# Performance work log

Measured on AMD Instinct MI355X. Metric: run time of the kernel, lower is better.

## Reference

```python
import jax, jax.numpy as jnp
import numpy as np

EPS = 1e-5   # epsilon default in the torch wrapper
D_CKV = 512  # latent-KV channels normalized by RMSNorm
D_ROPE = 64  # rope channels written to k_cache


def setup_inputs() -> dict:
    key = jax.random.key(0)
    ks = jax.random.split(key, 5)
    B, S, L = 16, 1024, 8192
    kv = jax.random.normal(ks[0], (B, 1, S, D_CKV + D_ROPE), dtype=jnp.float32)
    gamma = jax.random.normal(ks[1], (D_CKV,), dtype=jnp.float32)
    cos = jax.random.normal(ks[2], (B, 1, S, D_ROPE), dtype=jnp.float32)
    sin = jax.random.normal(ks[3], (B, 1, S, D_ROPE), dtype=jnp.float32)
    index = jax.random.randint(ks[4], (B, S), 0, L, dtype=jnp.int32)
    k_cache = jnp.zeros((B, 1, L, D_ROPE), dtype=jnp.float32)
    ckv_cache = jnp.zeros((B, 1, L, D_CKV), dtype=jnp.float32)
    return {"kv": kv, "gamma": gamma, "cos": cos, "sin": sin,
            "index": index, "k_cache": k_cache, "ckv_cache": ckv_cache}


def reference(kv, gamma, cos, sin, index, k_cache, ckv_cache):
    # cacheMode='Norm': max_slot is the cache length dim
    B, _, S, D = kv.shape
    L = k_cache.shape[2]
    dr = k_cache.shape[3]            # 64 rope channels
    dc = D - dr                      # 512 latent channels

    idx = jnp.abs(index) % L         # [B, S], as in the torch wrapper

    ckv = kv[..., :dc]               # [B,1,S,512]
    kr = kv[..., dc:]                # [B,1,S,64]

    # RMSNorm over the 512 latent channels
    inv = jax.lax.rsqrt(jnp.mean(ckv * ckv, axis=-1, keepdims=True) + EPS)
    ckv_n = ckv * inv * gamma        # [B,1,S,512]

    # RoPE (rotate-half) on the 64 rope channels
    half = dr // 2
    rot = jnp.concatenate([-kr[..., half:], kr[..., :half]], axis=-1)
    k_r = kr * cos + rot * sin       # [B,1,S,64]

    # scatter-write each token into its cache slot (per batch)
    gidx = (jnp.arange(B, dtype=idx.dtype)[:, None] * L + idx).reshape(-1)  # [B*S]
    k_new = k_cache.reshape(B * L, dr).at[gidx].set(k_r.reshape(B * S, dr)).reshape(B, 1, L, dr)
    ckv_new = ckv_cache.reshape(B * L, dc).at[gidx].set(ckv_n.reshape(B * S, dc)).reshape(B, 1, L, dc)
    return k_new, ckv_new
```

## Files before the change

kernel.cpp:

```cpp
#include <hip/hip_runtime.h>

#define B_  16
#define S_  1024
#define L_  8192
#define DC  512
#define DR  64
#define EPSV 1e-5f

typedef float fv4 __attribute__((ext_vector_type(4)));

__global__ void owner_kernel(const int* __restrict__ index, int* __restrict__ owner) {
    int t = blockIdx.x * blockDim.x + threadIdx.x;
    if (t >= B_ * S_) return;
    int b = t >> 10;
    int s = t & (S_ - 1);
    int v = index[t];
    v = v < 0 ? -v : v;
    int idx = v & (L_ - 1);
    atomicMax(&owner[b * L_ + idx], s);
}

__global__ __launch_bounds__(256) void update_kernel(
    const float* __restrict__ kv,
    const float* __restrict__ gamma,
    const float* __restrict__ cosb,
    const float* __restrict__ sinb,
    const float* __restrict__ k_cache,
    const float* __restrict__ ckv_cache,
    const int*  __restrict__ owner,
    float* __restrict__ out_k,
    float* __restrict__ out_ckv)
{
    const int wave = threadIdx.x >> 6;
    const int lane = threadIdx.x & 63;
    const int line = (blockIdx.x << 2) + wave;
    const int o = owner[line];

    fv4*   dst_ckv = (fv4*)(out_ckv + (size_t)line * DC);
    float* dst_k   = out_k + (size_t)line * DR;

    if (o < 0) {
        const fv4* src = (const fv4*)(ckv_cache + (size_t)line * DC);
        fv4 a = __builtin_nontemporal_load(&src[lane]);
        fv4 b = __builtin_nontemporal_load(&src[lane + 64]);
        __builtin_nontemporal_store(a, &dst_ckv[lane]);
        __builtin_nontemporal_store(b, &dst_ckv[lane + 64]);
        float kc = __builtin_nontemporal_load(&k_cache[(size_t)line * DR + lane]);
        __builtin_nontemporal_store(kc, &dst_k[lane]);
        return;
    }

    const int b = line >> 13;
    const int token = b * S_ + o;
    const float* kvp = kv + (size_t)token * (DC + DR);

    fv4 c0 = __builtin_nontemporal_load(&((const fv4*)kvp)[lane]);
    fv4 c1 = __builtin_nontemporal_load(&((const fv4*)kvp)[lane + 64]);
    const float kr = __builtin_nontemporal_load(&kvp[DC + lane]);
    const float cs = __builtin_nontemporal_load(&cosb[(size_t)token * DR + lane]);
    const float sn = __builtin_nontemporal_load(&sinb[(size_t)token * DR + lane]);

    float ss = c0.x*c0.x + c0.y*c0.y + c0.z*c0.z + c0.w*c0.w
             + c1.x*c1.x + c1.y*c1.y + c1.z*c1.z + c1.w*c1.w;
    #pragma unroll
    for (int off = 1; off < 64; off <<= 1)
        ss += __shfl_xor(ss, off);
    const float inv = rsqrtf(ss * (1.0f / DC) + EPSV);

    fv4 g0 = ((const fv4*)gamma)[lane];
    fv4 g1 = ((const fv4*)gamma)[lane + 64];
    fv4 r0 = c0 * inv * g0;
    fv4 r1 = c1 * inv * g1;
    __builtin_nontemporal_store(r0, &dst_ckv[lane]);
    __builtin_nontemporal_store(r1, &dst_ckv[lane + 64]);

    const float other = __shfl_xor(kr, 32);
    const float rot = (lane < 32) ? -other : other;
    __builtin_nontemporal_store(kr * cs + rot * sn, &dst_k[lane]);
}

extern "C" void kernel_launch(void* const* d_in, const int* in_sizes, int n_in,
                              void* d_out, int out_size, void* d_ws, size_t ws_size,
                              hipStream_t stream) {
    const float* kv        = (const float*)d_in[0];
    const float* gamma     = (const float*)d_in[1];
    const float* cosb      = (const float*)d_in[2];
    const float* sinb      = (const float*)d_in[3];
    const int*   index     = (const int*)d_in[4];
    const float* k_cache   = (const float*)d_in[5];
    const float* ckv_cache = (const float*)d_in[6];

    float* out_k   = (float*)d_out;
    float* out_ckv = out_k + (size_t)B_ * L_ * DR;

    int* owner = (int*)d_ws;

    owner_kernel<<<(B_ * S_ + 255) / 256, 256, 0, stream>>>(index, owner);

    update_kernel<<<(B_ * L_) / 4, 256, 0, stream>>>(
        kv, gamma, cosb, sinb, k_cache, ckv_cache, owner, out_k, out_ckv);
}
```

Measured before the change: 487.1 us.

## Replace per-slot gather with bulk cache memcpy plus per-token scatter

Instead of one kernel that visits every cache slot and either copies the old cache line or computes the owning token's result, the outputs are first filled with two device-to-device memcpys of the caches. A new scatter kernel then launches one wave per token, skips tokens that are not the last writer for their slot, and writes the RMSNorm and RoPE results into place. This drops the per-line owner branching and lets a tuned copy engine handle the bulk data. In exchange it reads the full caches even for slots that get overwritten, writes those slots twice, and adds launch and serialization points.

```diff
diff --git a/kernel.cpp b/kernel.cpp
--- a/kernel.cpp
+++ b/kernel.cpp
@@ -20,45 +20,34 @@
     atomicMax(&owner[b * L_ + idx], s);
 }
 
-__global__ __launch_bounds__(256) void update_kernel(
+__global__ __launch_bounds__(256) void scatter_kernel(
     const float* __restrict__ kv,
     const float* __restrict__ gamma,
     const float* __restrict__ cosb,
     const float* __restrict__ sinb,
-    const float* __restrict__ k_cache,
-    const float* __restrict__ ckv_cache,
+    const int*  __restrict__ index,
     const int*  __restrict__ owner,
     float* __restrict__ out_k,
     float* __restrict__ out_ckv)
 {
     const int wave = threadIdx.x >> 6;
     const int lane = threadIdx.x & 63;
-    const int line = (blockIdx.x << 2) + wave;
-    const int o = owner[line];
+    const int t = (blockIdx.x << 2) + wave;
+    const int b = t >> 10;
+    const int s = t & (S_ - 1);
 
-    fv4*   dst_ckv = (fv4*)(out_ckv + (size_t)line * DC);
-    float* dst_k   = out_k + (size_t)line * DR;
+    int v = index[t];
+    v = v < 0 ? -v : v;
+    const int line = b * L_ + (v & (L_ - 1));
+    if (owner[line] != s) return;
 
-    if (o < 0) {
-        const fv4* src = (const fv4*)(ckv_cache + (size_t)line * DC);
-        fv4 a = __builtin_nontemporal_load(&src[lane]);
-        fv4 b = __builtin_nontemporal_load(&src[lane + 64]);
-        __builtin_nontemporal_store(a, &dst_ckv[lane]);
-        __builtin_nontemporal_store(b, &dst_ckv[lane + 64]);
-        float kc = __builtin_nontemporal_load(&k_cache[(size_t)line * DR + lane]);
-        __builtin_nontemporal_store(kc, &dst_k[lane]);
-        return;
-    }
-
-    const int b = line >> 13;
-    const int token = b * S_ + o;
-    const float* kvp = kv + (size_t)token * (DC + DR);
+    const float* kvp = kv + (size_t)t * (DC + DR);
 
     fv4 c0 = __builtin_nontemporal_load(&((const fv4*)kvp)[lane]);
     fv4 c1 = __builtin_nontemporal_load(&((const fv4*)kvp)[lane + 64]);
     const float kr = __builtin_nontemporal_load(&kvp[DC + lane]);
-    const float cs = __builtin_nontemporal_load(&cosb[(size_t)token * DR + lane]);
-    const float sn = __builtin_nontemporal_load(&sinb[(size_t)token * DR + lane]);
+    const float cs = __builtin_nontemporal_load(&cosb[(size_t)t * DR + lane]);
+    const float sn = __builtin_nontemporal_load(&sinb[(size_t)t * DR + lane]);
 
     float ss = c0.x*c0.x + c0.y*c0.y + c0.z*c0.z + c0.w*c0.w
              + c1.x*c1.x + c1.y*c1.y + c1.z*c1.z + c1.w*c1.w;
@@ -71,12 +60,13 @@
     fv4 g1 = ((const fv4*)gamma)[lane + 64];
     fv4 r0 = c0 * inv * g0;
     fv4 r1 = c1 * inv * g1;
+    fv4* dst_ckv = (fv4*)(out_ckv + (size_t)line * DC);
     __builtin_nontemporal_store(r0, &dst_ckv[lane]);
     __builtin_nontemporal_store(r1, &dst_ckv[lane + 64]);
 
     const float other = __shfl_xor(kr, 32);
     const float rot = (lane < 32) ? -other : other;
-    __builtin_nontemporal_store(kr * cs + rot * sn, &dst_k[lane]);
+    __builtin_nontemporal_store(kr * cs + rot * sn, &out_k[(size_t)line * DR + lane]);
 }
 
 extern "C" void kernel_launch(void* const* d_in, const int* in_sizes, int n_in,
@@ -95,8 +85,13 @@
 
     int* owner = (int*)d_ws;
 
-    owner_kernel<<<(B_ * S_ + 255) / 256, 256, 0, stream>>>(index, owner);
+    owner_kernel<<<(B_ * S_) / 256, 256, 0, stream>>>(index, owner);
 
-    update_kernel<<<(B_ * L_) / 4, 256, 0, stream>>>(
-        kv, gamma, cosb, sinb, k_cache, ckv_cache, owner, out_k, out_ckv);
+    hipMemcpyAsync(out_k, k_cache, (size_t)B_ * L_ * DR * sizeof(float),
+                   hipMemcpyDeviceToDevice, stream);
+    hipMemcpyAsync(out_ckv, ckv_cache, (size_t)B_ * L_ * DC * sizeof(float),
+                   hipMemcpyDeviceToDevice, stream);
+
+    scatter_kernel<<<(B_ * S_) / 4, 256, 0, stream>>>(
+        kv, gamma, cosb, sinb, index, owner, out_k, out_ckv);
 }
```

After: 525.9 us. 8.0% more time.
